# Kernel optimization log

Hardware: AMD Instinct MI355X
Metric: run time of the kernel (lower is better)

## Reference

```python
import jax, jax.numpy as jnp
import numpy as np

N = 50000      # nodes
E = 600000     # edges
D = 128        # inp_dim == emb_dim
R = 100        # num_rels
B = 4          # num_bases
L = 2          # num_layers
EPS = 1e-5


def setup_inputs() -> dict:
    key = jax.random.key(0)
    ks = jax.random.split(key, 4 + 6 * L)
    inp = {
        "feat": jax.random.normal(ks[0], (N, D), dtype=jnp.float32),
        "src": jax.random.randint(ks[1], (E,), 0, N),
        "dst": jax.random.randint(ks[2], (E,), 0, N),
        "etype": jax.random.randint(ks[3], (E,), 0, R),
    }
    for l in range(L):
        o = 4 + 6 * l
        s = 1.0 / np.sqrt(D)
        inp[f"V{l}"] = jax.random.normal(ks[o + 0], (B, D, D), dtype=jnp.float32) * s
        inp[f"comb{l}"] = jax.random.normal(ks[o + 1], (R, B), dtype=jnp.float32)
        inp[f"loop{l}"] = jax.random.normal(ks[o + 2], (D, D), dtype=jnp.float32) * s
        inp[f"bias{l}"] = jax.random.normal(ks[o + 3], (D,), dtype=jnp.float32) * 0.01
        inp[f"gamma{l}"] = jnp.ones((D,), dtype=jnp.float32)
        inp[f"beta{l}"] = jnp.zeros((D,), dtype=jnp.float32)
    return inp


def _rel_graph_conv(x, src, dst, etype, V, comb, W_loop, bias):
    # basis-decomposed relational conv: W_r = sum_b comb[r,b] * V[b]
    xb = jnp.einsum('nd,bdo->nbo', x, V)            # [N, B, D] project onto bases once
    msg = jnp.einsum('ebo,eb->eo', xb[src], comb[etype])  # [E, D] per-edge typed message
    agg = jax.ops.segment_sum(msg, dst, num_segments=N)   # scatter-add to destinations
    h = agg + x @ W_loop + bias                     # self-loop + bias (DGL defaults)
    return jax.nn.relu(h)


def _batch_norm(h, gamma, beta):
    mu = jnp.mean(h, axis=0)
    var = jnp.mean(jnp.square(h - mu), axis=0)      # biased var (training-mode BN)
    return gamma * (h - mu) * jax.lax.rsqrt(var + EPS) + beta


def reference(feat, src, dst, etype,
              V0, comb0, loop0, bias0, gamma0, beta0,
              V1, comb1, loop1, bias1, gamma1, beta1):
    h = feat
    h = _rel_graph_conv(h, src, dst, etype, V0, comb0, loop0, bias0)
    h = _batch_norm(h, gamma0, beta0)
    h = _rel_graph_conv(h, src, dst, etype, V1, comb1, loop1, bias1)
    h = _batch_norm(h, gamma1, beta1)
    return h  # JK='last'
```

## Files before the change

kernel.cpp:

```cpp
#include <hip/hip_runtime.h>
#include <hip/hip_bf16.h>

#define Nn 50000
#define Ee 600000
#define Dd 128
#define EPSc 1e-5f
#define GX 391
#define NB 196

typedef unsigned int u32;
typedef unsigned short u16;
typedef short s16x8 __attribute__((ext_vector_type(8)));
typedef float f32x4 __attribute__((ext_vector_type(4)));

__device__ inline float bf2f(u32 lo16) { return __uint_as_float(lo16 << 16); }
__device__ inline u16 f2bf(float f) {
    u32 b = __float_as_uint(f);
    return (u16)((b + 0x7fffu + ((b >> 16) & 1u)) >> 16);
}
__device__ inline void gload16(const void* g, void* l) {
    __builtin_amdgcn_global_load_lds(
        (const __attribute__((address_space(1))) u32*)g,
        (__attribute__((address_space(3))) u32*)l, 16, 0, 0);
}

__global__ __launch_bounds__(256) void hist_k(const int* __restrict__ dst,
                                              int* __restrict__ cnt) {
    int e = blockIdx.x * 256 + threadIdx.x;
    if (e < Ee) atomicAdd(&cnt[dst[e]], 1);
}

__global__ __launch_bounds__(256) void scanA_k(const int* __restrict__ cnt,
                                               int* __restrict__ rowp,
                                               int* __restrict__ bsum) {
    __shared__ int ws4[4];
    const int tid = threadIdx.x, lane = tid & 63, w = tid >> 6;
    const int i = blockIdx.x * 256 + tid;
    int v = (i < Nn) ? cnt[i] : 0;
    int incl = v;
#pragma unroll
    for (int off = 1; off < 64; off <<= 1) {
        int u = __shfl_up(incl, off, 64);
        if (lane >= off) incl += u;
    }
    if (lane == 63) ws4[w] = incl;
    __syncthreads();
    if (tid == 0) {
        int run = 0;
#pragma unroll
        for (int j = 0; j < 4; j++) { int s = ws4[j]; ws4[j] = run; run += s; }
    }
    __syncthreads();
    incl += ws4[w];
    if (i < Nn) rowp[i + 1] = incl;
    if (tid == 255) bsum[blockIdx.x] = incl;
}

__global__ __launch_bounds__(256) void scanB_k(const int* __restrict__ bsum,
                                               int* __restrict__ boff) {
    __shared__ int ws4[4];
    const int tid = threadIdx.x, lane = tid & 63, w = tid >> 6;
    int v = (tid < NB) ? bsum[tid] : 0;
    int incl = v;
#pragma unroll
    for (int off = 1; off < 64; off <<= 1) {
        int u = __shfl_up(incl, off, 64);
        if (lane >= off) incl += u;
    }
    if (lane == 63) ws4[w] = incl;
    __syncthreads();
    if (tid == 0) {
        int run = 0;
#pragma unroll
        for (int j = 0; j < 4; j++) { int s = ws4[j]; ws4[j] = run; run += s; }
    }
    __syncthreads();
    if (tid < NB) boff[tid] = incl + ws4[w] - v;
}

__global__ __launch_bounds__(256) void scanC_k(const int* __restrict__ boff,
                                               int* __restrict__ rowp) {
    const int i = blockIdx.x * 256 + threadIdx.x;
    if (i < Nn) rowp[i + 1] += boff[blockIdx.x];
    if (i == 0) rowp[0] = 0;
}

__global__ __launch_bounds__(256) void scatter_k(const int* __restrict__ src,
                                                 const int* __restrict__ dst,
                                                 const int* __restrict__ et,
                                                 int* __restrict__ cursor,
                                                 int2* __restrict__ se) {
    int e = blockIdx.x * 256 + threadIdx.x;
    if (e < Ee) {
        int pos = atomicAdd(&cursor[dst[e]], 1);
        se[pos] = make_int2(src[e], et[e]);
    }
}

__global__ __launch_bounds__(256) void conv_k(const float* __restrict__ in,
                                              u16* __restrict__ out) {
    const int total = Nn * 32;
    for (int i = blockIdx.x * 256 + threadIdx.x; i < total; i += gridDim.x * 256) {
        float4 v = ((const float4*)in)[i];
        ((ushort4*)out)[i] = make_ushort4(f2bf(v.x), f2bf(v.y), f2bf(v.z), f2bf(v.w));
    }
}

__global__ __launch_bounds__(256) void wprep_k(const float* __restrict__ V,
                                               const float* __restrict__ loop,
                                               u16* __restrict__ Wt) {
    int i = blockIdx.x * 256 + threadIdx.x;
    if (i >= 128 * 640) return;
    int c = i / 640, k = i - c * 640;
    float v = (k < 512) ? V[(size_t)k * 128 + c] : loop[(size_t)(k - 512) * 128 + c];
    Wt[i] = f2bf(v);
}

__global__ __launch_bounds__(256) void agg_k(const u16* __restrict__ x16,
                                             const int2* __restrict__ se,
                                             const int* __restrict__ rowp,
                                             const float* __restrict__ comb,
                                             u16* __restrict__ yb16) {
    const int node = blockIdx.x * 4 + (threadIdx.x >> 6);
    const int lane = threadIdx.x & 63;
    const int beg = rowp[node], end = rowp[node + 1];
    float a0x = 0.f, a0y = 0.f, a1x = 0.f, a1y = 0.f;
    float a2x = 0.f, a2y = 0.f, a3x = 0.f, a3y = 0.f;
    const int eL = end - 1;
    const u32 co = (u32)lane * 2u;

    for (int e0 = beg; e0 < end; e0 += 8) {
        const int m = end - e0;
        int2 rc[8];
        u32 xv[8];
#pragma unroll
        for (int j = 0; j < 8; j++) rc[j] = se[min(e0 + j, eL)];
#pragma unroll
        for (int j = 0; j < 8; j++)
            xv[j] = *(const u32*)&x16[(u32)rc[j].x * 128u + co];
#pragma unroll
        for (int j = 1; j < 8; j++)
            if (m <= j) xv[j] = 0;
#pragma unroll
        for (int j = 0; j < 8; j++) {
            const float4 c = ((const float4*)comb)[rc[j].y];
            const float fx = bf2f(xv[j] & 0xffffu);
            const float fy = bf2f(xv[j] >> 16);
            a0x += c.x * fx; a0y += c.x * fy;
            a1x += c.y * fx; a1y += c.y * fy;
            a2x += c.z * fx; a2y += c.z * fy;
            a3x += c.w * fx; a3y += c.w * fy;
        }
    }
    u32* yp = (u32*)(yb16 + (size_t)node * 512);
    yp[lane]       = (u32)f2bf(a0x) | ((u32)f2bf(a0y) << 16);
    yp[64 + lane]  = (u32)f2bf(a1x) | ((u32)f2bf(a1y) << 16);
    yp[128 + lane] = (u32)f2bf(a2x) | ((u32)f2bf(a2y) << 16);
    yp[192 + lane] = (u32)f2bf(a3x) | ((u32)f2bf(a3y) << 16);
}

__global__ __launch_bounds__(256) void gemm_mfma_k(const u16* __restrict__ yb16,
                                                   const u16* __restrict__ x16,
                                                   const u16* __restrict__ Wt,
                                                   const float* __restrict__ bias,
                                                   float* __restrict__ OUT,
                                                   float* __restrict__ partials) {
    __shared__ __align__(16) char As[8192];
    __shared__ __align__(16) char Bs[8192];
    const int tid = threadIdx.x;
    const int lane = tid & 63, wid = tid >> 6;
    const int wr = wid >> 1, wc = wid & 1;
    const int bm = blockIdx.x * 128;

    f32x4 acc[4][4] = {};

    const int r0 = wid * 32;
    const int lrow = lane >> 2;
    const int sphys = lane & 3;
    const int rowL0 = r0 + lrow, rowL1 = r0 + 16 + lrow;
    const int slog0 = (sphys ^ ((rowL0 >> 1) & 3)) * 8;
    const int slog1 = (sphys ^ ((rowL1 >> 1) & 3)) * 8;
    int ga0 = bm + rowL0; if (ga0 >= Nn) ga0 = Nn - 1;
    int ga1 = bm + rowL1; if (ga1 >= Nn) ga1 = Nn - 1;

    for (int k0 = 0; k0 < 640; k0 += 32) {
        __syncthreads();
        const u16 *as0, *as1;
        if (k0 < 512) {
            as0 = yb16 + (size_t)ga0 * 512 + k0 + slog0;
            as1 = yb16 + (size_t)ga1 * 512 + k0 + slog1;
        } else {
            as0 = x16 + (size_t)ga0 * 128 + (k0 - 512) + slog0;
            as1 = x16 + (size_t)ga1 * 128 + (k0 - 512) + slog1;
        }
        gload16(as0, &As[r0 * 64]);
        gload16(as1, &As[(r0 + 16) * 64]);
        gload16(Wt + (size_t)rowL0 * 640 + k0 + slog0, &Bs[r0 * 64]);
        gload16(Wt + (size_t)rowL1 * 640 + k0 + slog1, &Bs[(r0 + 16) * 64]);
        __syncthreads();
        s16x8 a[4], b[4];
#pragma unroll
        for (int m = 0; m < 4; m++) {
            int row = wr * 64 + m * 16 + (lane & 15);
            a[m] = *(const s16x8*)&As[row * 64 + (((lane >> 4) ^ ((row >> 1) & 3)) << 4)];
            int col = wc * 64 + m * 16 + (lane & 15);
            b[m] = *(const s16x8*)&Bs[col * 64 + (((lane >> 4) ^ ((col >> 1) & 3)) << 4)];
        }
#pragma unroll
        for (int m = 0; m < 4; m++)
#pragma unroll
            for (int n = 0; n < 4; n++)
                acc[m][n] = __builtin_amdgcn_mfma_f32_16x16x32_bf16(a[m], b[n],
                                                                    acc[m][n], 0, 0, 0);
    }
    float bv[4], cs[4] = {}, cq[4] = {};
#pragma unroll
    for (int n = 0; n < 4; n++) bv[n] = bias[wc * 64 + n * 16 + (lane & 15)];
#pragma unroll
    for (int m = 0; m < 4; m++) {
        const int rb = bm + wr * 64 + m * 16 + ((lane >> 4) << 2);
#pragma unroll
        for (int e = 0; e < 4; e++) {
            const int r = rb + e;
            if (r < Nn) {
                float* op = OUT + (size_t)r * 128 + wc * 64 + (lane & 15);
#pragma unroll
                for (int n = 0; n < 4; n++) {
                    float v = fmaxf(acc[m][n][e] + bv[n], 0.f);
                    op[n * 16] = v;
                    cs[n] += v;
                    cq[n] += v * v;
                }
            }
        }
    }
#pragma unroll
    for (int n = 0; n < 4; n++) {
        cs[n] += __shfl_xor(cs[n], 16);
        cs[n] += __shfl_xor(cs[n], 32);
        cq[n] += __shfl_xor(cq[n], 16);
        cq[n] += __shfl_xor(cq[n], 32);
    }
    __syncthreads();
    float* red = (float*)As;
    if (wr == 1 && lane < 16) {
#pragma unroll
        for (int n = 0; n < 4; n++) {
            const int col = wc * 64 + n * 16 + lane;
            red[col] = cs[n];
            red[128 + col] = cq[n];
        }
    }
    __syncthreads();
    if (wr == 0 && lane < 16) {
        float* pp = partials + (size_t)blockIdx.x * 256;
#pragma unroll
        for (int n = 0; n < 4; n++) {
            const int col = wc * 64 + n * 16 + lane;
            pp[col] = cs[n] + red[col];
            pp[128 + col] = cq[n] + red[128 + col];
        }
    }
}

__global__ __launch_bounds__(256) void red_k(const float* __restrict__ partials,
                                             float* __restrict__ stats) {
    const int c = threadIdx.x;
    float s = 0.f;
    for (int b = blockIdx.x; b < GX; b += gridDim.x)
        s += partials[(size_t)b * 256 + c];
    unsafeAtomicAdd(&stats[c], s);
}

__global__ __launch_bounds__(256) void norm_k(const float* __restrict__ h,
                                              const float* __restrict__ stats,
                                              const float* __restrict__ gamma,
                                              const float* __restrict__ beta,
                                              float* __restrict__ out,
                                              u16* __restrict__ xb) {
    const float invN = 1.0f / (float)Nn;
    int total = Nn * 32;
    for (int i = blockIdx.x * blockDim.x + threadIdx.x; i < total;
         i += gridDim.x * blockDim.x) {
        int c = (i & 31) * 4;
        float4 v = ((const float4*)h)[i];
        float4 o;
        {
            float mu = stats[c + 0] * invN;
            float var = stats[Dd + c + 0] * invN - mu * mu;
            o.x = gamma[c + 0] * (v.x - mu) * rsqrtf(var + EPSc) + beta[c + 0];
        }
        {
            float mu = stats[c + 1] * invN;
            float var = stats[Dd + c + 1] * invN - mu * mu;
            o.y = gamma[c + 1] * (v.y - mu) * rsqrtf(var + EPSc) + beta[c + 1];
        }
        {
            float mu = stats[c + 2] * invN;
            float var = stats[Dd + c + 2] * invN - mu * mu;
            o.z = gamma[c + 2] * (v.z - mu) * rsqrtf(var + EPSc) + beta[c + 2];
        }
        {
            float mu = stats[c + 3] * invN;
            float var = stats[Dd + c + 3] * invN - mu * mu;
            o.w = gamma[c + 3] * (v.w - mu) * rsqrtf(var + EPSc) + beta[c + 3];
        }
        ((float4*)out)[i] = o;
        if (xb) ((ushort4*)xb)[i] = make_ushort4(f2bf(o.x), f2bf(o.y),
                                                 f2bf(o.z), f2bf(o.w));
    }
}

extern "C" void kernel_launch(void* const* d_in, const int* in_sizes, int n_in,
                              void* d_out, int out_size, void* d_ws, size_t ws_size,
                              hipStream_t stream) {
    const float* feat = (const float*)d_in[0];
    const int* src = (const int*)d_in[1];
    const int* dst = (const int*)d_in[2];
    const int* et = (const int*)d_in[3];
    float* out = (float*)d_out;

    char* p = (char*)d_ws;
    u16* yb16 = (u16*)p;     p += (size_t)Nn * 512 * 2;
    u16* x16 = (u16*)p;      p += (size_t)Nn * 128 * 2;
    u16* Wt = (u16*)p;       p += (size_t)128 * 640 * 2;
    int* rowp = (int*)p;     p += ((((size_t)(Nn + 1) * 4) + 15) & ~15ull);
    int2* se = (int2*)p;     p += (size_t)Ee * 8;
    float* partials = (float*)p;  p += (size_t)GX * 256 * 4;
    float* stats = (float*)p;     p += 2 * Dd * 4;
    int* bsum = (int*)p;          p += ((NB * 4 + 15) & ~15);
    int* boff = (int*)p;          p += ((NB * 4 + 15) & ~15);
    int* cursor = (int*)yb16;

    hipMemsetAsync(cursor, 0, (size_t)Nn * 4, stream);
    hist_k<<<(Ee + 255) / 256, 256, 0, stream>>>(dst, cursor);
    scanA_k<<<NB, 256, 0, stream>>>(cursor, rowp, bsum);
    scanB_k<<<1, 256, 0, stream>>>(bsum, boff);
    scanC_k<<<NB, 256, 0, stream>>>(boff, rowp);
    hipMemcpyAsync(cursor, rowp, (size_t)Nn * 4, hipMemcpyDeviceToDevice, stream);
    scatter_k<<<(Ee + 255) / 256, 256, 0, stream>>>(src, dst, et, cursor, se);
    conv_k<<<1024, 256, 0, stream>>>(feat, x16);

    for (int l = 0; l < 2; l++) {
        const float* V = (const float*)d_in[4 + 6 * l + 0];
        const float* comb = (const float*)d_in[4 + 6 * l + 1];
        const float* loop = (const float*)d_in[4 + 6 * l + 2];
        const float* bias = (const float*)d_in[4 + 6 * l + 3];
        const float* gamma = (const float*)d_in[4 + 6 * l + 4];
        const float* beta = (const float*)d_in[4 + 6 * l + 5];

        wprep_k<<<(128 * 640 + 255) / 256, 256, 0, stream>>>(V, loop, Wt);
        agg_k<<<(Nn + 3) / 4, 256, 0, stream>>>(x16, se, rowp, comb, yb16);
        hipMemsetAsync(stats, 0, 2 * Dd * sizeof(float), stream);
        gemm_mfma_k<<<GX, 256, 0, stream>>>(yb16, x16, Wt, bias, out, partials);
        red_k<<<8, 256, 0, stream>>>(partials, stats);
        norm_k<<<2048, 256, 0, stream>>>(out, stats, gamma, beta, out,
                                         (l == 0) ? x16 : nullptr);
    }
}
```

Baseline: 292.8 us.

## Process two nodes per wave in aggregation and trim launches and copies

The aggregation kernel now has each wavefront handle two destination nodes at once, with four edges each per step, to expose more independent gathers. The cursor copy is folded into the scan kernel, both layers' weight prep is merged into one launch before the loop, and the stats memset and atomics are replaced by a single-block deterministic reduction. Layer 0 normalisation no longer writes the fp32 output, only the bf16 copy. These changes cut launch count and memory traffic, but pairing nodes makes each wave run to the larger of the two degrees and spends registers on the second accumulator set.

```diff
diff --git a/kernel.cpp b/kernel.cpp
--- a/kernel.cpp
+++ b/kernel.cpp
@@ -79,10 +79,15 @@
 }
 
 __global__ __launch_bounds__(256) void scanC_k(const int* __restrict__ boff,
-                                               int* __restrict__ rowp) {
+                                               int* __restrict__ rowp,
+                                               int* __restrict__ cursor) {
     const int i = blockIdx.x * 256 + threadIdx.x;
-    if (i < Nn) rowp[i + 1] += boff[blockIdx.x];
-    if (i == 0) rowp[0] = 0;
+    if (i < Nn) {
+        int v = rowp[i + 1] + boff[blockIdx.x];
+        rowp[i + 1] = v;
+        if (i + 1 < Nn) cursor[i + 1] = v;
+    }
+    if (i == 0) { rowp[0] = 0; cursor[0] = 0; }
 }
 
 __global__ __launch_bounds__(256) void scatter_k(const int* __restrict__ src,
@@ -106,13 +111,18 @@
     }
 }
 
-__global__ __launch_bounds__(256) void wprep_k(const float* __restrict__ V,
-                                               const float* __restrict__ loop,
-                                               u16* __restrict__ Wt) {
+__global__ __launch_bounds__(256) void wprep2_k(const float* __restrict__ V0,
+                                                const float* __restrict__ loop0,
+                                                const float* __restrict__ V1,
+                                                const float* __restrict__ loop1,
+                                                u16* __restrict__ Wt) {
     int i = blockIdx.x * 256 + threadIdx.x;
-    if (i >= 128 * 640) return;
-    int c = i / 640, k = i - c * 640;
-    float v = (k < 512) ? V[(size_t)k * 128 + c] : loop[(size_t)(k - 512) * 128 + c];
+    if (i >= 2 * 128 * 640) return;
+    int l = i / 81920, r = i - l * 81920;
+    int c = r / 640, k = r - c * 640;
+    const float* V = l ? V1 : V0;
+    const float* lp = l ? loop1 : loop0;
+    float v = (k < 512) ? V[(size_t)k * 128 + c] : lp[(size_t)(k - 512) * 128 + c];
     Wt[i] = f2bf(v);
 }
 
@@ -121,42 +131,72 @@
                                              const int* __restrict__ rowp,
                                              const float* __restrict__ comb,
                                              u16* __restrict__ yb16) {
-    const int node = blockIdx.x * 4 + (threadIdx.x >> 6);
+    const int wv = threadIdx.x >> 6;
     const int lane = threadIdx.x & 63;
-    const int beg = rowp[node], end = rowp[node + 1];
-    float a0x = 0.f, a0y = 0.f, a1x = 0.f, a1y = 0.f;
-    float a2x = 0.f, a2y = 0.f, a3x = 0.f, a3y = 0.f;
-    const int eL = end - 1;
+    const int nA = blockIdx.x * 8 + wv * 2;
+    const int begA = rowp[nA], endA = rowp[nA + 1], endB = rowp[nA + 2];
+    const int begB = endA;
+    const int eLA = endA - 1, eLB = endB - 1;
     const u32 co = (u32)lane * 2u;
 
-    for (int e0 = beg; e0 < end; e0 += 8) {
-        const int m = end - e0;
+    float A0x = 0.f, A0y = 0.f, A1x = 0.f, A1y = 0.f;
+    float A2x = 0.f, A2y = 0.f, A3x = 0.f, A3y = 0.f;
+    float B0x = 0.f, B0y = 0.f, B1x = 0.f, B1y = 0.f;
+    float B2x = 0.f, B2y = 0.f, B3x = 0.f, B3y = 0.f;
+
+    const int degA = endA - begA, degB = endB - begB;
+    const int nst = (max(degA, degB) + 3) >> 2;
+
+    for (int s = 0; s < nst; s++) {
+        const int eA = begA + s * 4, eB = begB + s * 4;
+        const int mA = endA - eA, mB = endB - eB;
         int2 rc[8];
         u32 xv[8];
 #pragma unroll
-        for (int j = 0; j < 8; j++) rc[j] = se[min(e0 + j, eL)];
+        for (int j = 0; j < 4; j++) {
+            rc[j]     = se[(mA > 0) ? min(eA + j, eLA) : 0];
+            rc[4 + j] = se[(mB > 0) ? min(eB + j, eLB) : 0];
+        }
 #pragma unroll
         for (int j = 0; j < 8; j++)
-            xv[j] = *(const u32*)&x16[(u32)rc[j].x * 128u + co];
-#pragma unroll
-        for (int j = 1; j < 8; j++)
-            if (m <= j) xv[j] = 0;
-#pragma unroll
-        for (int j = 0; j < 8; j++) {
-            const float4 c = ((const float4*)comb)[rc[j].y];
-            const float fx = bf2f(xv[j] & 0xffffu);
-            const float fy = bf2f(xv[j] >> 16);
-            a0x += c.x * fx; a0y += c.x * fy;
-            a1x += c.y * fx; a1y += c.y * fy;
-            a2x += c.z * fx; a2y += c.z * fy;
-            a3x += c.w * fx; a3y += c.w * fy;
-        }
-    }
-    u32* yp = (u32*)(yb16 + (size_t)node * 512);
-    yp[lane]       = (u32)f2bf(a0x) | ((u32)f2bf(a0y) << 16);
-    yp[64 + lane]  = (u32)f2bf(a1x) | ((u32)f2bf(a1y) << 16);
-    yp[128 + lane] = (u32)f2bf(a2x) | ((u32)f2bf(a2y) << 16);
-    yp[192 + lane] = (u32)f2bf(a3x) | ((u32)f2bf(a3y) << 16);
+            xv[j] = *(const u32*)&x16[(size_t)(u32)rc[j].x * 128 + co];
+#pragma unroll
+        for (int j = 0; j < 4; j++) {
+            if (j >= mA) xv[j] = 0;
+            if (j >= mB) xv[4 + j] = 0;
+        }
+#pragma unroll
+        for (int j = 0; j < 4; j++) {
+            {
+                const float4 c = ((const float4*)comb)[rc[j].y];
+                const float fx = bf2f(xv[j] & 0xffffu);
+                const float fy = bf2f(xv[j] >> 16);
+                A0x += c.x * fx; A0y += c.x * fy;
+                A1x += c.y * fx; A1y += c.y * fy;
+                A2x += c.z * fx; A2y += c.z * fy;
+                A3x += c.w * fx; A3y += c.w * fy;
+            }
+            {
+                const float4 c = ((const float4*)comb)[rc[4 + j].y];
+                const float fx = bf2f(xv[4 + j] & 0xffffu);
+                const float fy = bf2f(xv[4 + j] >> 16);
+                B0x += c.x * fx; B0y += c.x * fy;
+                B1x += c.y * fx; B1y += c.y * fy;
+                B2x += c.z * fx; B2y += c.z * fy;
+                B3x += c.w * fx; B3y += c.w * fy;
+            }
+        }
+    }
+    u32* ypA = (u32*)(yb16 + (size_t)nA * 512);
+    ypA[lane]       = (u32)f2bf(A0x) | ((u32)f2bf(A0y) << 16);
+    ypA[64 + lane]  = (u32)f2bf(A1x) | ((u32)f2bf(A1y) << 16);
+    ypA[128 + lane] = (u32)f2bf(A2x) | ((u32)f2bf(A2y) << 16);
+    ypA[192 + lane] = (u32)f2bf(A3x) | ((u32)f2bf(A3y) << 16);
+    u32* ypB = ypA + 256;
+    ypB[lane]       = (u32)f2bf(B0x) | ((u32)f2bf(B0y) << 16);
+    ypB[64 + lane]  = (u32)f2bf(B1x) | ((u32)f2bf(B1y) << 16);
+    ypB[128 + lane] = (u32)f2bf(B2x) | ((u32)f2bf(B2y) << 16);
+    ypB[192 + lane] = (u32)f2bf(B3x) | ((u32)f2bf(B3y) << 16);
 }
 
 __global__ __launch_bounds__(256) void gemm_mfma_k(const u16* __restrict__ yb16,
@@ -266,17 +306,23 @@
 __global__ __launch_bounds__(256) void red_k(const float* __restrict__ partials,
                                              float* __restrict__ stats) {
     const int c = threadIdx.x;
-    float s = 0.f;
-    for (int b = blockIdx.x; b < GX; b += gridDim.x)
-        s += partials[(size_t)b * 256 + c];
-    unsafeAtomicAdd(&stats[c], s);
+    float s0 = 0.f, s1 = 0.f, s2 = 0.f, s3 = 0.f;
+    int b = 0;
+    for (; b + 4 <= GX; b += 4) {
+        s0 += partials[(size_t)(b + 0) * 256 + c];
+        s1 += partials[(size_t)(b + 1) * 256 + c];
+        s2 += partials[(size_t)(b + 2) * 256 + c];
+        s3 += partials[(size_t)(b + 3) * 256 + c];
+    }
+    for (; b < GX; b++) s0 += partials[(size_t)b * 256 + c];
+    stats[c] = (s0 + s1) + (s2 + s3);
 }
 
 __global__ __launch_bounds__(256) void norm_k(const float* __restrict__ h,
                                               const float* __restrict__ stats,
                                               const float* __restrict__ gamma,
                                               const float* __restrict__ beta,
-                                              float* __restrict__ out,
+                                              float* __restrict__ outp,
                                               u16* __restrict__ xb) {
     const float invN = 1.0f / (float)Nn;
     int total = Nn * 32;
@@ -305,7 +351,7 @@
             float var = stats[Dd + c + 3] * invN - mu * mu;
             o.w = gamma[c + 3] * (v.w - mu) * rsqrtf(var + EPSc) + beta[c + 3];
         }
-        ((float4*)out)[i] = o;
+        if (outp) ((float4*)outp)[i] = o;
         if (xb) ((ushort4*)xb)[i] = make_ushort4(f2bf(o.x), f2bf(o.y),
                                                  f2bf(o.z), f2bf(o.w));
     }
@@ -323,7 +369,7 @@
     char* p = (char*)d_ws;
     u16* yb16 = (u16*)p;     p += (size_t)Nn * 512 * 2;
     u16* x16 = (u16*)p;      p += (size_t)Nn * 128 * 2;
-    u16* Wt = (u16*)p;       p += (size_t)128 * 640 * 2;
+    u16* Wt = (u16*)p;       p += (size_t)2 * 128 * 640 * 2;
     int* rowp = (int*)p;     p += ((((size_t)(Nn + 1) * 4) + 15) & ~15ull);
     int2* se = (int2*)p;     p += (size_t)Ee * 8;
     float* partials = (float*)p;  p += (size_t)GX * 256 * 4;
@@ -336,25 +382,25 @@
     hist_k<<<(Ee + 255) / 256, 256, 0, stream>>>(dst, cursor);
     scanA_k<<<NB, 256, 0, stream>>>(cursor, rowp, bsum);
     scanB_k<<<1, 256, 0, stream>>>(bsum, boff);
-    scanC_k<<<NB, 256, 0, stream>>>(boff, rowp);
-    hipMemcpyAsync(cursor, rowp, (size_t)Nn * 4, hipMemcpyDeviceToDevice, stream);
+    scanC_k<<<NB, 256, 0, stream>>>(boff, rowp, cursor);
     scatter_k<<<(Ee + 255) / 256, 256, 0, stream>>>(src, dst, et, cursor, se);
     conv_k<<<1024, 256, 0, stream>>>(feat, x16);
+    wprep2_k<<<(2 * 128 * 640 + 255) / 256, 256, 0, stream>>>(
+        (const float*)d_in[4], (const float*)d_in[6],
+        (const float*)d_in[10], (const float*)d_in[12], Wt);
 
     for (int l = 0; l < 2; l++) {
-        const float* V = (const float*)d_in[4 + 6 * l + 0];
         const float* comb = (const float*)d_in[4 + 6 * l + 1];
-        const float* loop = (const float*)d_in[4 + 6 * l + 2];
         const float* bias = (const float*)d_in[4 + 6 * l + 3];
         const float* gamma = (const float*)d_in[4 + 6 * l + 4];
         const float* beta = (const float*)d_in[4 + 6 * l + 5];
 
-        wprep_k<<<(128 * 640 + 255) / 256, 256, 0, stream>>>(V, loop, Wt);
-        agg_k<<<(Nn + 3) / 4, 256, 0, stream>>>(x16, se, rowp, comb, yb16);
-        hipMemsetAsync(stats, 0, 2 * Dd * sizeof(float), stream);
-        gemm_mfma_k<<<GX, 256, 0, stream>>>(yb16, x16, Wt, bias, out, partials);
-        red_k<<<8, 256, 0, stream>>>(partials, stats);
-        norm_k<<<2048, 256, 0, stream>>>(out, stats, gamma, beta, out,
+        agg_k<<<Nn / 8, 256, 0, stream>>>(x16, se, rowp, comb, yb16);
+        gemm_mfma_k<<<GX, 256, 0, stream>>>(yb16, x16, Wt + (size_t)l * 81920,
+                                            bias, out, partials);
+        red_k<<<1, 256, 0, stream>>>(partials, stats);
+        norm_k<<<2048, 256, 0, stream>>>(out, stats, gamma, beta,
+                                         (l == 0) ? nullptr : out,
                                          (l == 0) ? x16 : nullptr);
     }
 }
```

New measurement: 281.9 us. -3.7%, faster.
